# Optimization experiments

Measured on AMD Instinct MI355X. Metric: run time of the kernel, lower is better.

## Reference

```python
import jax, jax.numpy as jnp
import numpy as np

NUM_HEAD = 8
NUM_BOX = 4
K = 4                      # kernel_size
P = K * K                  # num_point
HEAD_DIM = 32
V_DIM = 256
Q_DIM = 256


def _kernel_indices():
    # even kernel: linspace(-K/2+0.5, K/2-0.5, K), stack (j, i) i.e. (x, y), /K
    idx = np.linspace(-K // 2 + 0.5, K // 2 - 0.5, K)
    i, j = np.meshgrid(idx, idx, indexing='ij')
    return jnp.asarray(np.stack([j, i], axis=-1).reshape(-1, 2) / K, dtype=jnp.float32)


def _bilinear(vm, gx, gy, Hf, Wf):
    # vm: [b,H,Hf*Wf,dh]; gx,gy: [b,H,M] normalized coords in [0,1]
    # grid_sample(2*g-1, align_corners=False, padding_mode='zeros') semantics
    x = gx * Wf - 0.5
    y = gy * Hf - 0.5
    x0 = jnp.floor(x)
    y0 = jnp.floor(y)
    wx1 = x - x0
    wy1 = y - y0

    def corner(xi, yi, w):
        inb = (xi >= 0) & (xi < Wf) & (yi >= 0) & (yi < Hf)
        xi_c = jnp.clip(xi, 0, Wf - 1).astype(jnp.int32)
        yi_c = jnp.clip(yi, 0, Hf - 1).astype(jnp.int32)
        v = jnp.take_along_axis(vm, (yi_c * Wf + xi_c)[..., None], axis=2)
        return v * (w * inb)[..., None]

    return (corner(x0, y0, (1 - wx1) * (1 - wy1))
            + corner(x0 + 1, y0, wx1 * (1 - wy1))
            + corner(x0, y0 + 1, (1 - wx1) * wy1)
            + corner(x0 + 1, y0 + 1, wx1 * wy1))


def _forward(query, value, Hf, Wf, v_mask, v_valid_ratios, ref_windows,
             box_w, box_b, attn_w, attn_b, vproj_w, vproj_b, oproj_w, oproj_b):
    b, l1, _ = query.shape
    l2 = value.shape[1]
    ki = _kernel_indices()  # [P,2]

    value = value @ vproj_w.T + vproj_b
    value = jnp.where(v_mask[..., None], 0.0, value)
    vm = value.reshape(b, l2, NUM_HEAD, HEAD_DIM).transpose(0, 2, 1, 3)  # [b,H,l2,dh]

    off = (query @ box_w.T + box_b).reshape(b, l1, NUM_HEAD, NUM_BOX, 4)
    ref = ref_windows[:, :, None, None, :]                   # [b,l1,1,1,4]
    ref_size = ref[..., jnp.array([2, 3, 2, 3])]
    boxes = ref + off / 8.0 * ref_size                       # [b,l1,H,B,4]
    center = boxes[..., None, :2]
    size = boxes[..., None, 2:]
    grid = center + ki * jax.nn.relu(size)                   # [b,l1,H,B,P,2]
    grid = grid * v_valid_ratios

    # attention weights: [b,l1,H,B,2,2] -> repeat_interleave -> [b,l1,H,B,K,K]
    aw = (query @ attn_w.T + attn_b).reshape(b, l1, NUM_HEAD, NUM_BOX, 2, 2)
    aw = jnp.repeat(jnp.repeat(aw, K // 2, axis=-1), K // 2, axis=-2)
    spatial_w = jax.nn.softmax(aw.reshape(b, l1, NUM_HEAD, NUM_BOX * P), axis=-1)
    level_w = jax.nn.softmax(aw, axis=3).reshape(b, l1, NUM_HEAD, NUM_BOX * P)

    # per-head bilinear sampling at all B*P points per query
    g = grid.transpose(0, 2, 1, 3, 4, 5).reshape(b, NUM_HEAD, -1, 2)  # [b,H,l1*B*P,2]
    sampled = _bilinear(vm, g[..., 0], g[..., 1], Hf, Wf)             # [b,H,M,dh]
    sampled = sampled.reshape(b, NUM_HEAD, l1, NUM_BOX * P, HEAD_DIM)

    out = jnp.einsum('bhlpd,blhp->blhd', sampled, spatial_w).reshape(b, l1, V_DIM)
    output = out @ oproj_w.T + oproj_b
    # mask branch: level softmax (over boxes) weighted aggregate, summed over points
    mout = jnp.einsum('bhlpd,blhp->blhd', sampled, level_w).reshape(b, l1, V_DIM)
    mask_output = mout @ oproj_w.T + oproj_b
    return output, mask_output, aw


def setup_inputs() -> dict:
    key = jax.random.key(0)
    ks = jax.random.split(key, 12)
    b, l1, Hf, Wf = 8, 300, 64, 64
    l2 = Hf * Wf
    d = Q_DIM
    return {
        'query': jax.random.normal(ks[0], (b, l1, d), jnp.float32),
        'value': jax.random.normal(ks[1], (b, l2, V_DIM), jnp.float32),
        'v_shape': np.array([[Hf, Wf]], dtype=np.int64),
        'v_mask': jnp.zeros((b, l2), dtype=bool),
        'v_start_index': np.array([0], dtype=np.int64),
        'v_valid_ratios': jnp.ones((b, 1, 1, 1, 1, 2), jnp.float32),
        'ref_windows': jax.random.uniform(ks[2], (b, l1, 4), jnp.float32, 0.05, 0.6),
        'box_w': 0.02 * jax.random.normal(ks[3], (NUM_BOX * NUM_HEAD * 4, d), jnp.float32),
        'box_b': jax.random.uniform(ks[4], (NUM_HEAD * NUM_BOX * 4,), jnp.float32),
        'attn_w': 0.02 * jax.random.normal(ks[5], (NUM_HEAD * NUM_BOX * 4, d), jnp.float32),
        'attn_b': 0.1 * jax.random.normal(ks[6], (NUM_HEAD * NUM_BOX * 4,), jnp.float32),
        'vproj_w': 0.05 * jax.random.normal(ks[7], (V_DIM, V_DIM), jnp.float32),
        'vproj_b': jnp.zeros((V_DIM,), jnp.float32),
        'oproj_w': 0.05 * jax.random.normal(ks[8], (d, V_DIM), jnp.float32),
        'oproj_b': jnp.zeros((d,), jnp.float32),
    }


def reference(query, value, v_shape, v_mask, v_start_index, v_valid_ratios, ref_windows,
              box_w, box_b, attn_w, attn_b, vproj_w, vproj_b, oproj_w, oproj_b):
    Hf, Wf = int(v_shape[0, 0]), int(v_shape[0, 1])  # single level, static shapes
    return _forward(query, value, Hf, Wf, v_mask, v_valid_ratios, ref_windows,
                    box_w, box_b, attn_w, attn_b, vproj_w, vproj_b, oproj_w, oproj_b)
```

## Files before the change

### kernel.cpp

```cpp
#include <hip/hip_runtime.h>
#include <cstddef>

#define NH   8
#define NB   4
#define HD   32
#define NPIX 4096
#define NBATCH 8
#define NL   300
#define D    256
#define NQ   (NBATCH * NL)
#define NR   (2 * NQ)

typedef __attribute__((ext_vector_type(4))) float  f32x4;
typedef __attribute__((ext_vector_type(8))) short  bf16x8;

__device__ __forceinline__ unsigned short f2bf(float f) {
    union { float f; unsigned u; } v; v.f = f;
    unsigned r = v.u + 0x7fffu + ((v.u >> 16) & 1u);
    return (unsigned short)(r >> 16);
}

__device__ __forceinline__ bf16x8 pack8(const f32x4 a, const f32x4 b) {
    bf16x8 w;
    w[0] = (short)f2bf(a[0]); w[1] = (short)f2bf(a[1]);
    w[2] = (short)f2bf(a[2]); w[3] = (short)f2bf(a[3]);
    w[4] = (short)f2bf(b[0]); w[5] = (short)f2bf(b[1]);
    w[6] = (short)f2bf(b[2]); w[7] = (short)f2bf(b[3]);
    return w;
}

__global__ __launch_bounds__(256)
void vproj_mfma(const float* __restrict__ value, const float* __restrict__ W,
                const float* __restrict__ bias, const unsigned char* __restrict__ mask,
                float* __restrict__ vm)
{
    __shared__ short As[128][72];
    __shared__ short Bs[128][72];
    const int tid  = threadIdx.x;
    const int lane = tid & 63, wid = tid >> 6;
    const int wm = wid >> 1, wn = wid & 1;
    const int row0 = blockIdx.x * 128, col0 = blockIdx.y * 128;
    const int l16 = lane & 15, lg = lane >> 4;

    f32x4 acc[4][4] = {};

    const int ar = tid >> 1;
    const int ak = (tid & 1) * 32;

    for (int k0 = 0; k0 < D; k0 += 64) {
        const f32x4* pa = (const f32x4*)(value + (size_t)(row0 + ar) * D + k0 + ak);
        const f32x4* pb = (const f32x4*)(W     + (size_t)(col0 + ar) * D + k0 + ak);
        #pragma unroll
        for (int j = 0; j < 4; ++j) {
            *(bf16x8*)&As[ar][ak + j * 8] = pack8(pa[2 * j], pa[2 * j + 1]);
            *(bf16x8*)&Bs[ar][ak + j * 8] = pack8(pb[2 * j], pb[2 * j + 1]);
        }
        __syncthreads();
        #pragma unroll
        for (int kk = 0; kk < 2; ++kk) {
            bf16x8 af[4], bfr[4];
            #pragma unroll
            for (int m = 0; m < 4; ++m)
                af[m] = *(const bf16x8*)&As[wm * 64 + m * 16 + l16][kk * 32 + lg * 8];
            #pragma unroll
            for (int n = 0; n < 4; ++n)
                bfr[n] = *(const bf16x8*)&Bs[wn * 64 + n * 16 + l16][kk * 32 + lg * 8];
            #pragma unroll
            for (int m = 0; m < 4; ++m)
                #pragma unroll
                for (int n = 0; n < 4; ++n)
                    acc[m][n] = __builtin_amdgcn_mfma_f32_16x16x32_bf16(af[m], bfr[n], acc[m][n], 0, 0, 0);
        }
        __syncthreads();
    }
    #pragma unroll
    for (int m = 0; m < 4; ++m) {
        #pragma unroll
        for (int r = 0; r < 4; ++r) {
            const int grow = row0 + wm * 64 + m * 16 + lg * 4 + r;
            const int bb = grow >> 12, pix = grow & (NPIX - 1);
            const float mf = (mask[grow] != 0) ? 0.f : 1.f;
            #pragma unroll
            for (int n = 0; n < 4; ++n) {
                const int gcol = col0 + wn * 64 + n * 16 + l16;
                const int h = gcol >> 5, dd = gcol & 31;
                vm[((size_t)(bb * NH + h) * NPIX + pix) * HD + dd] = mf * (acc[m][n][r] + bias[gcol]);
            }
        }
    }
}

__global__ __launch_bounds__(256)
void proj_gemm(const float* __restrict__ query,
               const float* __restrict__ box_w, const float* __restrict__ box_b,
               const float* __restrict__ attn_w, const float* __restrict__ attn_b,
               float* __restrict__ bp, float* __restrict__ ap, float* __restrict__ awo)
{
    __shared__ float As[16][65];
    __shared__ float Bs[16][65];
    const int tid = threadIdx.x;
    const int tr = tid >> 4, tc = tid & 15;
    float acc[4][4] = {};
    const int row0 = blockIdx.x * 64, col0 = blockIdx.y * 64;
    for (int k0 = 0; k0 < D; k0 += 16) {
        #pragma unroll
        for (int i = 0; i < 4; ++i) {
            int idx = tid + i * 256;
            int r = idx >> 4, kk = idx & 15;
            int qrow = min(row0 + r, NQ - 1);
            As[kk][r] = query[(size_t)qrow * D + k0 + kk];
            int c256 = col0 + r;
            const float* src = (c256 < 128) ? (box_w + (size_t)c256 * D)
                                            : (attn_w + (size_t)(c256 - 128) * D);
            Bs[kk][r] = src[k0 + kk];
        }
        __syncthreads();
        #pragma unroll
        for (int kk = 0; kk < 16; ++kk) {
            float a[4], bv[4];
            #pragma unroll
            for (int i = 0; i < 4; ++i) a[i] = As[kk][tr * 4 + i];
            #pragma unroll
            for (int j = 0; j < 4; ++j) bv[j] = Bs[kk][tc * 4 + j];
            #pragma unroll
            for (int i = 0; i < 4; ++i)
                #pragma unroll
                for (int j = 0; j < 4; ++j)
                    acc[i][j] += a[i] * bv[j];
        }
        __syncthreads();
    }
    #pragma unroll
    for (int i = 0; i < 4; ++i) {
        int q = row0 + tr * 4 + i;
        if (q >= NQ) continue;
        #pragma unroll
        for (int j = 0; j < 4; ++j) {
            int col = col0 + tc * 4 + j;
            if (col < 128) {
                bp[(size_t)q * 128 + col] = acc[i][j] + box_b[col];
            } else {
                int rc = col - 128;
                float val = acc[i][j] + attn_b[rc];
                ap[(size_t)q * 128 + rc] = val;
                int h = rc >> 4, bx = (rc >> 2) & 3, rr = (rc >> 1) & 1, cc = rc & 1;
                float* awq = awo + (size_t)q * 512 + (size_t)(h * NB + bx) * 16;
                awq[(2 * rr + 0) * 4 + 2 * cc + 0] = val;
                awq[(2 * rr + 0) * 4 + 2 * cc + 1] = val;
                awq[(2 * rr + 1) * 4 + 2 * cc + 0] = val;
                awq[(2 * rr + 1) * 4 + 2 * cc + 1] = val;
            }
        }
    }
}

__global__ __launch_bounds__(256)
void sample_kernel(const float* __restrict__ vm, const float* __restrict__ bp,
                   const float* __restrict__ ap, const float* __restrict__ ref_windows,
                   const float* __restrict__ vratio, const int* __restrict__ vshape,
                   float* __restrict__ outp, float* __restrict__ moutp)
{
    __shared__ float sbp[128], sap[128], sref[4];
    const int blk = blockIdx.x;
    const int tid = threadIdx.x;
    const int bb = blk / NL;
    const int h = tid >> 5, dd = tid & 31;
    if (tid < 128) { sbp[tid] = bp[(size_t)blk * 128 + tid]; sap[tid] = ap[(size_t)blk * 128 + tid]; }
    if (tid < 4) sref[tid] = ref_windows[(size_t)blk * 4 + tid];
    __syncthreads();
    const int Hf = vshape[0], Wf = vshape[1];
    const float Hff = (float)Hf, Wff = (float)Wf;
    const float vr0 = vratio[bb * 2 + 0], vr1 = vratio[bb * 2 + 1];

    float aw16[16];
    #pragma unroll
    for (int k = 0; k < 16; ++k) aw16[k] = sap[h * 16 + k];
    float mx = aw16[0];
    #pragma unroll
    for (int k = 1; k < 16; ++k) mx = fmaxf(mx, aw16[k]);
    float e16[16]; float ssum = 0.f;
    #pragma unroll
    for (int k = 0; k < 16; ++k) { e16[k] = expf(aw16[k] - mx); ssum += e16[k]; }
    ssum *= 4.0f;
    float ld[4];
    #pragma unroll
    for (int c = 0; c < 4; ++c) ld[c] = e16[c] + e16[4 + c] + e16[8 + c] + e16[12 + c];

    const float kidx[4] = {-0.375f, -0.125f, 0.125f, 0.375f};
    float acc = 0.f, accm = 0.f;
    const float* vmh = vm + ((size_t)(bb * NH + h) * NPIX) * HD + dd;

    #pragma unroll
    for (int box = 0; box < NB; ++box) {
        const float o0 = sbp[h * 16 + box * 4 + 0];
        const float o1 = sbp[h * 16 + box * 4 + 1];
        const float o2 = sbp[h * 16 + box * 4 + 2];
        const float o3 = sbp[h * 16 + box * 4 + 3];
        const float cx  = sref[0] + o0 * 0.125f * sref[2];
        const float cy  = sref[1] + o1 * 0.125f * sref[3];
        const float bw_ = sref[2] + o2 * 0.125f * sref[2];
        const float bh_ = sref[3] + o3 * 0.125f * sref[3];
        const float rw = fmaxf(bw_, 0.f), rh = fmaxf(bh_, 0.f);
        #pragma unroll
        for (int ii = 0; ii < 4; ++ii) {
            const float gy = (cy + kidx[ii] * rh) * vr1;
            const float y = gy * Hff - 0.5f;
            const float y0f = floorf(y);
            const int iy0 = (int)y0f;
            const float wy1 = y - y0f, wy0 = 1.f - wy1;
            #pragma unroll
            for (int jj = 0; jj < 4; ++jj) {
                const float gx = (cx + kidx[jj] * rw) * vr0;
                const float x = gx * Wff - 0.5f;
                const float x0f = floorf(x);
                const int ix0 = (int)x0f;
                const float wx1 = x - x0f, wx0 = 1.f - wx1;
                float samp = 0.f;
                #pragma unroll
                for (int cyi = 0; cyi < 2; ++cyi) {
                    const int yi = iy0 + cyi;
                    const float wy = cyi ? wy1 : wy0;
                    const bool yin = (yi >= 0) && (yi < Hf);
                    const int yc = min(max(yi, 0), Hf - 1);
                    #pragma unroll
                    for (int cxi = 0; cxi < 2; ++cxi) {
                        const int xi = ix0 + cxi;
                        const float wx = cxi ? wx1 : wx0;
                        const bool xin = (xi >= 0) && (xi < Wf);
                        const int xc = min(max(xi, 0), Wf - 1);
                        const float wgt = (yin && xin) ? (wy * wx) : 0.f;
                        const float v = vmh[(size_t)(yc * Wf + xc) * HD];
                        samp += v * wgt;
                    }
                }
                const int kpos = (ii >> 1) * 2 + (jj >> 1);
                const float ev = e16[box * 4 + kpos];
                acc  += samp * (ev / ssum);
                accm += samp * (ev / ld[kpos]);
            }
        }
    }
    outp[(size_t)blk * 256 + h * 32 + dd]  = acc;
    moutp[(size_t)blk * 256 + h * 32 + dd] = accm;
}

__global__ __launch_bounds__(512)
void oproj_mfma(const float* __restrict__ R, const float* __restrict__ W,
                const float* __restrict__ bias, float* __restrict__ Out)
{
    __shared__ short As[128][72];
    __shared__ short Bs[256][72];
    const int tid  = threadIdx.x;
    const int lane = tid & 63, wid = tid >> 6;
    const int wm = wid >> 2, wn = wid & 3;
    const int row0 = blockIdx.x * 128;
    const int l16 = lane & 15, lg = lane >> 4;

    f32x4 acc[4][4] = {};

    const int arr = tid >> 2;
    const int ark = (tid & 3) * 16;
    const int brr = tid >> 1;
    const int brk = (tid & 1) * 32;

    for (int k0 = 0; k0 < D; k0 += 64) {
        const int arow = min(row0 + arr, NR - 1);
        const f32x4* pa = (const f32x4*)(R + (size_t)arow * D + k0 + ark);
        #pragma unroll
        for (int j = 0; j < 2; ++j)
            *(bf16x8*)&As[arr][ark + j * 8] = pack8(pa[2 * j], pa[2 * j + 1]);
        const f32x4* pb = (const f32x4*)(W + (size_t)brr * D + k0 + brk);
        #pragma unroll
        for (int j = 0; j < 4; ++j)
            *(bf16x8*)&Bs[brr][brk + j * 8] = pack8(pb[2 * j], pb[2 * j + 1]);
        __syncthreads();
        #pragma unroll
        for (int kk = 0; kk < 2; ++kk) {
            bf16x8 af[4], bfr[4];
            #pragma unroll
            for (int m = 0; m < 4; ++m)
                af[m] = *(const bf16x8*)&As[wm * 64 + m * 16 + l16][kk * 32 + lg * 8];
            #pragma unroll
            for (int n = 0; n < 4; ++n)
                bfr[n] = *(const bf16x8*)&Bs[wn * 64 + n * 16 + l16][kk * 32 + lg * 8];
            #pragma unroll
            for (int m = 0; m < 4; ++m)
                #pragma unroll
                for (int n = 0; n < 4; ++n)
                    acc[m][n] = __builtin_amdgcn_mfma_f32_16x16x32_bf16(af[m], bfr[n], acc[m][n], 0, 0, 0);
        }
        __syncthreads();
    }
    #pragma unroll
    for (int m = 0; m < 4; ++m) {
        #pragma unroll
        for (int r = 0; r < 4; ++r) {
            const int grow = row0 + wm * 64 + m * 16 + lg * 4 + r;
            if (grow >= NR) continue;
            #pragma unroll
            for (int n = 0; n < 4; ++n) {
                const int gcol = wn * 64 + n * 16 + l16;
                Out[(size_t)grow * D + gcol] = acc[m][n][r] + bias[gcol];
            }
        }
    }
}

extern "C" void kernel_launch(void* const* d_in, const int* in_sizes, int n_in,
                              void* d_out, int out_size, void* d_ws, size_t ws_size,
                              hipStream_t stream)
{
    const float* query        = (const float*)d_in[0];
    const float* value        = (const float*)d_in[1];
    const int*   vshape       = (const int*)d_in[2];
    const unsigned char* vmask= (const unsigned char*)d_in[3];
    const float* vratio       = (const float*)d_in[5];
    const float* refw         = (const float*)d_in[6];
    const float* box_w        = (const float*)d_in[7];
    const float* box_b        = (const float*)d_in[8];
    const float* attn_w       = (const float*)d_in[9];
    const float* attn_b       = (const float*)d_in[10];
    const float* vproj_w      = (const float*)d_in[11];
    const float* vproj_b      = (const float*)d_in[12];
    const float* oproj_w      = (const float*)d_in[13];
    const float* oproj_b      = (const float*)d_in[14];

    float* ws = (float*)d_ws;
    float* vm = ws;
    float* bp = vm + 8388608;
    float* ap = bp + 307200;

    float* out1 = (float*)d_out;
    float* out2 = out1 + 614400;
    float* awo  = out2 + 614400;

    float* outp  = out1;
    float* moutp = out2;

    vproj_mfma<<<dim3(256, 2), 256, 0, stream>>>(value, vproj_w, vproj_b, vmask, vm);
    proj_gemm<<<dim3(38, 4), 256, 0, stream>>>(query, box_w, box_b, attn_w, attn_b, bp, ap, awo);
    sample_kernel<<<NQ, 256, 0, stream>>>(vm, bp, ap, refw, vratio, vshape, outp, moutp);
    oproj_mfma<<<38, 512, 0, stream>>>(out1, oproj_w, oproj_b, out1);
}
```

Measured before the change: 239.5 us.

## Store projected values in bf16, pre-convert GEMM inputs, precompute sampling tables

Adds a separate pass that converts value and the projection weight to bf16. The value-projection GEMM then reads bf16 operands straight from global memory without LDS and writes its output as bf16, halving the bytes the sampling kernel has to gather. The sampling kernel now builds per-point offset, bilinear-weight and softmax-scale tables in shared memory once per query, instead of every thread recomputing them. The cost is an extra kernel launch and conversion pass, plus lower precision in the sampled values.

New measurement: 216.0 us. -9.8%, faster.

```diff
diff --git a/kernel.cpp b/kernel.cpp
--- a/kernel.cpp
+++ b/kernel.cpp
@@ -19,7 +19,9 @@
     unsigned r = v.u + 0x7fffu + ((v.u >> 16) & 1u);
     return (unsigned short)(r >> 16);
 }
-
+__device__ __forceinline__ float bf2f(unsigned short u) {
+    union { unsigned u; float f; } v; v.u = ((unsigned)u) << 16; return v.f;
+}
 __device__ __forceinline__ bf16x8 pack8(const f32x4 a, const f32x4 b) {
     bf16x8 w;
     w[0] = (short)f2bf(a[0]); w[1] = (short)f2bf(a[1]);
@@ -30,61 +32,65 @@
 }
 
 __global__ __launch_bounds__(256)
-void vproj_mfma(const float* __restrict__ value, const float* __restrict__ W,
+void tobf16_kernel(const float* __restrict__ value, const float* __restrict__ W,
+                   unsigned short* __restrict__ vb, unsigned short* __restrict__ wb)
+{
+    const int i = blockIdx.x * 256 + threadIdx.x;
+    {
+        const size_t off = (size_t)i * 8;
+        f32x4 a = *(const f32x4*)(value + off);
+        f32x4 b = *(const f32x4*)(value + off + 4);
+        *(bf16x8*)(vb + off) = pack8(a, b);
+    }
+    if (i < 8192) {
+        const size_t off = (size_t)i * 8;
+        f32x4 a = *(const f32x4*)(W + off);
+        f32x4 b = *(const f32x4*)(W + off + 4);
+        *(bf16x8*)(wb + off) = pack8(a, b);
+    }
+}
+
+__global__ __launch_bounds__(256)
+void vproj_mfma(const unsigned short* __restrict__ Vb, const unsigned short* __restrict__ Wb,
                 const float* __restrict__ bias, const unsigned char* __restrict__ mask,
-                float* __restrict__ vm)
-{
-    __shared__ short As[128][72];
-    __shared__ short Bs[128][72];
+                unsigned short* __restrict__ vm)
+{
     const int tid  = threadIdx.x;
     const int lane = tid & 63, wid = tid >> 6;
     const int wm = wid >> 1, wn = wid & 1;
-    const int row0 = blockIdx.x * 128, col0 = blockIdx.y * 128;
+    const int row0 = blockIdx.x * 64;
     const int l16 = lane & 15, lg = lane >> 4;
 
-    f32x4 acc[4][4] = {};
-
-    const int ar = tid >> 1;
-    const int ak = (tid & 1) * 32;
-
-    for (int k0 = 0; k0 < D; k0 += 64) {
-        const f32x4* pa = (const f32x4*)(value + (size_t)(row0 + ar) * D + k0 + ak);
-        const f32x4* pb = (const f32x4*)(W     + (size_t)(col0 + ar) * D + k0 + ak);
-        #pragma unroll
-        for (int j = 0; j < 4; ++j) {
-            *(bf16x8*)&As[ar][ak + j * 8] = pack8(pa[2 * j], pa[2 * j + 1]);
-            *(bf16x8*)&Bs[ar][ak + j * 8] = pack8(pb[2 * j], pb[2 * j + 1]);
-        }
-        __syncthreads();
-        #pragma unroll
-        for (int kk = 0; kk < 2; ++kk) {
-            bf16x8 af[4], bfr[4];
-            #pragma unroll
-            for (int m = 0; m < 4; ++m)
-                af[m] = *(const bf16x8*)&As[wm * 64 + m * 16 + l16][kk * 32 + lg * 8];
-            #pragma unroll
-            for (int n = 0; n < 4; ++n)
-                bfr[n] = *(const bf16x8*)&Bs[wn * 64 + n * 16 + l16][kk * 32 + lg * 8];
-            #pragma unroll
-            for (int m = 0; m < 4; ++m)
-                #pragma unroll
-                for (int n = 0; n < 4; ++n)
-                    acc[m][n] = __builtin_amdgcn_mfma_f32_16x16x32_bf16(af[m], bfr[n], acc[m][n], 0, 0, 0);
-        }
-        __syncthreads();
-    }
-    #pragma unroll
-    for (int m = 0; m < 4; ++m) {
+    f32x4 acc[2][8] = {};
+    const unsigned short* pa0 = Vb + (size_t)(row0 + wm * 32 + l16) * D + lg * 8;
+    const unsigned short* pb0 = Wb + (size_t)(wn * 128 + l16) * D + lg * 8;
+
+    #pragma unroll
+    for (int ks = 0; ks < 8; ++ks) {
+        bf16x8 af[2], bfr[8];
+        #pragma unroll
+        for (int m = 0; m < 2; ++m) af[m]  = *(const bf16x8*)(pa0 + (size_t)m * 16 * D + ks * 32);
+        #pragma unroll
+        for (int n = 0; n < 8; ++n) bfr[n] = *(const bf16x8*)(pb0 + (size_t)n * 16 * D + ks * 32);
+        #pragma unroll
+        for (int m = 0; m < 2; ++m)
+            #pragma unroll
+            for (int n = 0; n < 8; ++n)
+                acc[m][n] = __builtin_amdgcn_mfma_f32_16x16x32_bf16(af[m], bfr[n], acc[m][n], 0, 0, 0);
+    }
+    #pragma unroll
+    for (int m = 0; m < 2; ++m) {
         #pragma unroll
         for (int r = 0; r < 4; ++r) {
-            const int grow = row0 + wm * 64 + m * 16 + lg * 4 + r;
+            const int grow = row0 + wm * 32 + m * 16 + lg * 4 + r;
             const int bb = grow >> 12, pix = grow & (NPIX - 1);
             const float mf = (mask[grow] != 0) ? 0.f : 1.f;
             #pragma unroll
-            for (int n = 0; n < 4; ++n) {
-                const int gcol = col0 + wn * 64 + n * 16 + l16;
+            for (int n = 0; n < 8; ++n) {
+                const int gcol = wn * 128 + n * 16 + l16;
                 const int h = gcol >> 5, dd = gcol & 31;
-                vm[((size_t)(bb * NH + h) * NPIX + pix) * HD + dd] = mf * (acc[m][n][r] + bias[gcol]);
+                vm[((size_t)(bb * NH + h) * NPIX + pix) * HD + dd] =
+                    f2bf(mf * (acc[m][n][r] + bias[gcol]));
             }
         }
     }
@@ -155,93 +161,96 @@
 }
 
 __global__ __launch_bounds__(256)
-void sample_kernel(const float* __restrict__ vm, const float* __restrict__ bp,
+void sample_kernel(const unsigned short* __restrict__ vm, const float* __restrict__ bp,
                    const float* __restrict__ ap, const float* __restrict__ ref_windows,
                    const float* __restrict__ vratio, const int* __restrict__ vshape,
                    float* __restrict__ outp, float* __restrict__ moutp)
 {
-    __shared__ float sbp[128], sap[128], sref[4];
-    const int blk = blockIdx.x;
-    const int tid = threadIdx.x;
+    __shared__ float sbp[128], sap[128], swh[128], lwh[128], sref4[4];
+    __shared__ float4 boxdat[32];
+    __shared__ int4   O4[512];
+    __shared__ float4 W4[512];
+    __shared__ float2 SL[512];
+    const int blk = blockIdx.x, tid = threadIdx.x;
     const int bb = blk / NL;
-    const int h = tid >> 5, dd = tid & 31;
     if (tid < 128) { sbp[tid] = bp[(size_t)blk * 128 + tid]; sap[tid] = ap[(size_t)blk * 128 + tid]; }
-    if (tid < 4) sref[tid] = ref_windows[(size_t)blk * 4 + tid];
+    if (tid < 4) sref4[tid] = ref_windows[(size_t)blk * 4 + tid];
     __syncthreads();
     const int Hf = vshape[0], Wf = vshape[1];
     const float Hff = (float)Hf, Wff = (float)Wf;
     const float vr0 = vratio[bb * 2 + 0], vr1 = vratio[bb * 2 + 1];
 
-    float aw16[16];
-    #pragma unroll
-    for (int k = 0; k < 16; ++k) aw16[k] = sap[h * 16 + k];
-    float mx = aw16[0];
-    #pragma unroll
-    for (int k = 1; k < 16; ++k) mx = fmaxf(mx, aw16[k]);
-    float e16[16]; float ssum = 0.f;
-    #pragma unroll
-    for (int k = 0; k < 16; ++k) { e16[k] = expf(aw16[k] - mx); ssum += e16[k]; }
-    ssum *= 4.0f;
-    float ld[4];
-    #pragma unroll
-    for (int c = 0; c < 4; ++c) ld[c] = e16[c] + e16[4 + c] + e16[8 + c] + e16[12 + c];
+    if (tid < 128) {
+        float a = sap[tid];
+        float m = a;
+        m = fmaxf(m, __shfl_xor(m, 1));
+        m = fmaxf(m, __shfl_xor(m, 2));
+        m = fmaxf(m, __shfl_xor(m, 4));
+        m = fmaxf(m, __shfl_xor(m, 8));
+        float e = expf(a - m);
+        float ldv = e + __shfl_xor(e, 4);
+        ldv += __shfl_xor(ldv, 8);
+        float ss = ldv + __shfl_xor(ldv, 1);
+        ss += __shfl_xor(ss, 2);
+        swh[tid] = e / (4.f * ss);
+        lwh[tid] = e / ldv;
+    } else if (tid < 160) {
+        int j = tid - 128;
+        float o0 = sbp[j * 4 + 0], o1 = sbp[j * 4 + 1];
+        float o2 = sbp[j * 4 + 2], o3 = sbp[j * 4 + 3];
+        float cx = sref4[0] + o0 * 0.125f * sref4[2];
+        float cy = sref4[1] + o1 * 0.125f * sref4[3];
+        float rw = fmaxf(sref4[2] + o2 * 0.125f * sref4[2], 0.f);
+        float rh = fmaxf(sref4[3] + o3 * 0.125f * sref4[3], 0.f);
+        boxdat[j] = make_float4(cx, cy, rw, rh);
+    }
+    __syncthreads();
 
     const float kidx[4] = {-0.375f, -0.125f, 0.125f, 0.375f};
+    #pragma unroll
+    for (int pp = 0; pp < 2; ++pp) {
+        const int p = tid + pp * 256;
+        const float4 bd = boxdat[p >> 4];
+        const int ii = (p >> 2) & 3, jj = p & 3;
+        const float gy = (bd.y + kidx[ii] * bd.w) * vr1;
+        const float gx = (bd.x + kidx[jj] * bd.z) * vr0;
+        const float y = gy * Hff - 0.5f, x = gx * Wff - 0.5f;
+        const float y0f = floorf(y), x0f = floorf(x);
+        const int iy0 = (int)y0f, ix0 = (int)x0f;
+        const float wy1 = y - y0f, wx1 = x - x0f;
+        const float wy0 = 1.f - wy1, wx0 = 1.f - wx1;
+        const bool y0in = (iy0 >= 0) & (iy0 < Hf);
+        const bool y1in = (iy0 + 1 >= 0) & (iy0 + 1 < Hf);
+        const bool x0in = (ix0 >= 0) & (ix0 < Wf);
+        const bool x1in = (ix0 + 1 >= 0) & (ix0 + 1 < Wf);
+        const int yc0 = min(max(iy0, 0), Hf - 1), yc1 = min(max(iy0 + 1, 0), Hf - 1);
+        const int xc0 = min(max(ix0, 0), Wf - 1), xc1 = min(max(ix0 + 1, 0), Wf - 1);
+        O4[p] = make_int4((yc0 * Wf + xc0) * HD, (yc0 * Wf + xc1) * HD,
+                          (yc1 * Wf + xc0) * HD, (yc1 * Wf + xc1) * HD);
+        W4[p] = make_float4((y0in & x0in) ? wy0 * wx0 : 0.f,
+                            (y0in & x1in) ? wy0 * wx1 : 0.f,
+                            (y1in & x0in) ? wy1 * wx0 : 0.f,
+                            (y1in & x1in) ? wy1 * wx1 : 0.f);
+        const int kpos = ((p >> 2) & 2) | ((p >> 1) & 1);
+        const int hk = (p >> 6) * 16 + ((p >> 4) & 3) * 4 + kpos;
+        SL[p] = make_float2(swh[hk], lwh[hk]);
+    }
+    __syncthreads();
+
+    const int h = tid >> 5, dd = tid & 31;
+    const unsigned short* base = vm + ((size_t)(bb * NH + h) * NPIX) * HD + dd;
     float acc = 0.f, accm = 0.f;
-    const float* vmh = vm + ((size_t)(bb * NH + h) * NPIX) * HD + dd;
-
-    #pragma unroll
-    for (int box = 0; box < NB; ++box) {
-        const float o0 = sbp[h * 16 + box * 4 + 0];
-        const float o1 = sbp[h * 16 + box * 4 + 1];
-        const float o2 = sbp[h * 16 + box * 4 + 2];
-        const float o3 = sbp[h * 16 + box * 4 + 3];
-        const float cx  = sref[0] + o0 * 0.125f * sref[2];
-        const float cy  = sref[1] + o1 * 0.125f * sref[3];
-        const float bw_ = sref[2] + o2 * 0.125f * sref[2];
-        const float bh_ = sref[3] + o3 * 0.125f * sref[3];
-        const float rw = fmaxf(bw_, 0.f), rh = fmaxf(bh_, 0.f);
-        #pragma unroll
-        for (int ii = 0; ii < 4; ++ii) {
-            const float gy = (cy + kidx[ii] * rh) * vr1;
-            const float y = gy * Hff - 0.5f;
-            const float y0f = floorf(y);
-            const int iy0 = (int)y0f;
-            const float wy1 = y - y0f, wy0 = 1.f - wy1;
-            #pragma unroll
-            for (int jj = 0; jj < 4; ++jj) {
-                const float gx = (cx + kidx[jj] * rw) * vr0;
-                const float x = gx * Wff - 0.5f;
-                const float x0f = floorf(x);
-                const int ix0 = (int)x0f;
-                const float wx1 = x - x0f, wx0 = 1.f - wx1;
-                float samp = 0.f;
-                #pragma unroll
-                for (int cyi = 0; cyi < 2; ++cyi) {
-                    const int yi = iy0 + cyi;
-                    const float wy = cyi ? wy1 : wy0;
-                    const bool yin = (yi >= 0) && (yi < Hf);
-                    const int yc = min(max(yi, 0), Hf - 1);
-                    #pragma unroll
-                    for (int cxi = 0; cxi < 2; ++cxi) {
-                        const int xi = ix0 + cxi;
-                        const float wx = cxi ? wx1 : wx0;
-                        const bool xin = (xi >= 0) && (xi < Wf);
-                        const int xc = min(max(xi, 0), Wf - 1);
-                        const float wgt = (yin && xin) ? (wy * wx) : 0.f;
-                        const float v = vmh[(size_t)(yc * Wf + xc) * HD];
-                        samp += v * wgt;
-                    }
-                }
-                const int kpos = (ii >> 1) * 2 + (jj >> 1);
-                const float ev = e16[box * 4 + kpos];
-                acc  += samp * (ev / ssum);
-                accm += samp * (ev / ld[kpos]);
-            }
-        }
-    }
-    outp[(size_t)blk * 256 + h * 32 + dd]  = acc;
-    moutp[(size_t)blk * 256 + h * 32 + dd] = accm;
+    #pragma unroll 4
+    for (int t = 0; t < 64; ++t) {
+        const int p = h * 64 + t;
+        const int4 o = O4[p]; const float4 w = W4[p]; const float2 sl = SL[p];
+        const float samp = bf2f(base[o.x]) * w.x + bf2f(base[o.y]) * w.y
+                         + bf2f(base[o.z]) * w.z + bf2f(base[o.w]) * w.w;
+        acc  += samp * sl.x;
+        accm += samp * sl.y;
+    }
+    outp[(size_t)blk * 256 + tid]  = acc;
+    moutp[(size_t)blk * 256 + tid] = accm;
 }
 
 __global__ __launch_bounds__(512)
@@ -257,7 +266,6 @@
     const int l16 = lane & 15, lg = lane >> 4;
 
     f32x4 acc[4][4] = {};
-
     const int arr = tid >> 2;
     const int ark = (tid & 3) * 16;
     const int brr = tid >> 1;
@@ -325,9 +333,10 @@
     const float* oproj_w      = (const float*)d_in[13];
     const float* oproj_b      = (const float*)d_in[14];
 
-    float* ws = (float*)d_ws;
-    float* vm = ws;
-    float* bp = vm + 8388608;
+    unsigned short* vm_b  = (unsigned short*)d_ws;
+    unsigned short* val_b = vm_b + 8388608;
+    unsigned short* w_b   = val_b + 8388608;
+    float* bp = (float*)(w_b + 65536);
     float* ap = bp + 307200;
 
     float* out1 = (float*)d_out;
@@ -337,8 +346,9 @@
     float* outp  = out1;
     float* moutp = out2;
 
-    vproj_mfma<<<dim3(256, 2), 256, 0, stream>>>(value, vproj_w, vproj_b, vmask, vm);
+    tobf16_kernel<<<4096, 256, 0, stream>>>(value, vproj_w, val_b, w_b);
+    vproj_mfma<<<512, 256, 0, stream>>>(val_b, w_b, vproj_b, vmask, vm_b);
     proj_gemm<<<dim3(38, 4), 256, 0, stream>>>(query, box_w, box_b, attn_w, attn_b, bp, ap, awo);
-    sample_kernel<<<NQ, 256, 0, stream>>>(vm, bp, ap, refw, vratio, vshape, outp, moutp);
+    sample_kernel<<<NQ, 256, 0, stream>>>(vm_b, bp, ap, refw, vratio, vshape, outp, moutp);
     oproj_mfma<<<38, 512, 0, stream>>>(out1, oproj_w, oproj_b, out1);
 }
```
